# Kernel optimization log

Hardware: AMD Instinct MI355X
Metric: run time of the kernel (lower is better)

The kernel has to match this reference:

```python
import jax, jax.numpy as jnp
import numpy as np

T_MIN, T_MAX = 0.03, 0.34
STEPS = 32
K_MAX = 2
N_DIMS = 2  # homology dimensions [0, 1]

B, C, H, W = 128, 64, 64, 64
P = 128  # persistence pairs per (b, c)


def setup_inputs() -> dict:
    key = jax.random.key(0)
    k1, k2, k3, k4 = jax.random.split(key, 4)
    x = jax.random.uniform(k1, (B, C, H, W), dtype=jnp.float32)
    birth_idx = jax.random.randint(k2, (B, C, P), 0, H * W)
    death_idx = jax.random.randint(k3, (B, C, P), 0, H * W)
    pair_dim = jax.random.randint(k4, (B, C, P), 0, N_DIMS)
    return {"x": x, "birth_idx": birth_idx, "death_idx": death_idx, "pair_dim": pair_dim}


def reference(x, birth_idx, death_idx, pair_dim):
    # x: [B, C, H, W]; indices: [B, C, P] into flattened H*W grid.
    tseq = jnp.linspace(T_MIN, T_MAX, STEPS).astype(x.dtype)  # [T]
    b_, c_, h_, w_ = x.shape
    xf = x.reshape(b_, c_, h_ * w_)
    births = jnp.take_along_axis(xf, birth_idx, axis=-1)  # [B, C, P]
    deaths = jnp.take_along_axis(xf, death_idx, axis=-1)  # [B, C, P]
    # Landscape triangle functions: max(min(t - birth, death - t), 0) -> [B, C, P, T]
    tri = jnp.maximum(jnp.minimum(tseq - births[..., None], deaths[..., None] - tseq), 0.0)
    # Mask pairs by their homology dimension -> [B, C, D, P, T]
    dims = jnp.arange(N_DIMS)
    mask = pair_dim[:, :, None, :, None] == dims[None, None, :, None, None]
    land = jnp.where(mask, tri[:, :, None, :, :], 0.0)
    # Top-K_max landscapes over pairs, per (dim, t): original does -sort(-land)[:K]
    land_t = jnp.swapaxes(land, -1, -2)  # [B, C, D, T, P]
    top, _ = jax.lax.top_k(land_t, K_MAX)  # [B, C, D, T, K]
    return jnp.swapaxes(top, -1, -2)  # [B, C, D, K, T]
```

## Files before the change

### kernel.cpp

```cpp
#include <hip/hip_runtime.h>


constexpr int P = 128;
constexpr float T_MIN = 0.03f;
constexpr float T_MAX = 0.34f;
constexpr float BIG = 1e30f;

__global__ __launch_bounds__(256) void pl_topk_kernel(
    const float* __restrict__ x,
    const int* __restrict__ birth_idx,
    const int* __restrict__ death_idx,
    const int* __restrict__ pair_dim,
    float* __restrict__ out)
{
    __shared__ float2 tab[4][2][P];

    const int lane = threadIdx.x & 63;
    const int w = threadIdx.x >> 6;
    const int wid = blockIdx.x * 4 + w;

    const int d_lane = lane >> 5;
    const int t_idx = lane & 31;
    const float t = T_MIN + (T_MAX - T_MIN) * (float)t_idx * (1.0f / 31.0f);

    const long pbase = (long)wid * P;
    const int bi0 = birth_idx[pbase + lane];
    const int bi1 = birth_idx[pbase + 64 + lane];
    const int di0 = death_idx[pbase + lane];
    const int di1 = death_idx[pbase + 64 + lane];
    const int dm0 = pair_dim[pbase + lane];
    const int dm1 = pair_dim[pbase + 64 + lane];

    const long xbase = (long)wid * 4096;
    const float xb0 = x[xbase + bi0];
    const float xb1 = x[xbase + bi1];
    const float xd0 = x[xbase + di0];
    const float xd1 = x[xbase + di1];

    tab[w][dm0][lane]          = make_float2(xb0, xd0);
    tab[w][1 - dm0][lane]      = make_float2(BIG, -BIG);
    tab[w][dm1][64 + lane]     = make_float2(xb1, xd1);
    tab[w][1 - dm1][64 + lane] = make_float2(BIG, -BIG);

    __syncthreads();

    float m1 = 0.0f, m2 = 0.0f;
    const float2* tp = &tab[w][d_lane][0];
    #pragma unroll
    for (int p = 0; p < P; p += 2) {
        const float4 e = *reinterpret_cast<const float4*>(&tp[p]);
        const float v0 = fminf(t - e.x, e.y - t);
        const float v1 = fminf(t - e.z, e.w - t);
        m2 = fmaxf(m2, fminf(m1, v0));
        m1 = fmaxf(m1, v0);
        m2 = fmaxf(m2, fminf(m1, v1));
        m1 = fmaxf(m1, v1);
    }

    float* o = out + (long)wid * 128;
    o[d_lane * 64 + t_idx] = m1;
    o[d_lane * 64 + 32 + t_idx] = m2;
}

extern "C" void kernel_launch(void* const* d_in, const int* in_sizes, int n_in,
                              void* d_out, int out_size, void* d_ws, size_t ws_size,
                              hipStream_t stream) {
    const float* x = (const float*)d_in[0];
    const int* birth_idx = (const int*)d_in[1];
    const int* death_idx = (const int*)d_in[2];
    const int* pair_dim = (const int*)d_in[3];
    float* out = (float*)d_out;

    dim3 grid(2048), block(256);
    hipLaunchKernelGGL(pl_topk_kernel, grid, block, 0, stream,
                       x, birth_idx, death_idx, pair_dim, out);
}
```

Before: 27.23 us.

## Compact pairs per homology dimension with ballot prefix sums, drop block barrier

Pairs are no longer written into both dimension tables with sentinel padding. A wave ballot and popcount prefix sum now packs each dimension's pairs contiguously, so each half-wave scans only its own pairs (about half of P) instead of all P. The block-wide __syncthreads is replaced by an LDS waitcnt, which relies on each wave only reading its own slice. Index loads become int2 vector loads. The trade-off is a runtime loop bound with reduced unrolling and some extra ballot and popcount work. Correctness also depends on wave-level LDS ordering holding without a barrier.

```diff
diff --git a/kernel.cpp b/kernel.cpp
--- a/kernel.cpp
+++ b/kernel.cpp
@@ -13,7 +13,7 @@
     const int* __restrict__ pair_dim,
     float* __restrict__ out)
 {
-    __shared__ float2 tab[4][2][P];
+    __shared__ float2 tab[4][2][130];
 
     const int lane = threadIdx.x & 63;
     const int w = threadIdx.x >> 6;
@@ -24,30 +24,45 @@
     const float t = T_MIN + (T_MAX - T_MIN) * (float)t_idx * (1.0f / 31.0f);
 
     const long pbase = (long)wid * P;
-    const int bi0 = birth_idx[pbase + lane];
-    const int bi1 = birth_idx[pbase + 64 + lane];
-    const int di0 = death_idx[pbase + lane];
-    const int di1 = death_idx[pbase + 64 + lane];
-    const int dm0 = pair_dim[pbase + lane];
-    const int dm1 = pair_dim[pbase + 64 + lane];
+    const int2 bi = *reinterpret_cast<const int2*>(&birth_idx[pbase + 2 * lane]);
+    const int2 di = *reinterpret_cast<const int2*>(&death_idx[pbase + 2 * lane]);
+    const int2 dm = *reinterpret_cast<const int2*>(&pair_dim[pbase + 2 * lane]);
 
     const long xbase = (long)wid * 4096;
-    const float xb0 = x[xbase + bi0];
-    const float xb1 = x[xbase + bi1];
-    const float xd0 = x[xbase + di0];
-    const float xd1 = x[xbase + di1];
+    const float xb0 = x[xbase + bi.x];
+    const float xb1 = x[xbase + bi.y];
+    const float xd0 = x[xbase + di.x];
+    const float xd1 = x[xbase + di.y];
 
-    tab[w][dm0][lane]          = make_float2(xb0, xd0);
-    tab[w][1 - dm0][lane]      = make_float2(BIG, -BIG);
-    tab[w][dm1][64 + lane]     = make_float2(xb1, xd1);
-    tab[w][1 - dm1][64 + lane] = make_float2(BIG, -BIG);
+    const unsigned long long below = (lane == 63) ? ~0ull >> 1
+                                                  : (1ull << lane) - 1ull;
+    const unsigned long long a_d1 = __ballot(dm.x == 1);
+    const unsigned long long b_d1 = __ballot(dm.y == 1);
+    const unsigned long long a_d0 = ~a_d1;
+    const unsigned long long b_d0 = ~b_d1;
 
-    __syncthreads();
+    const int nA0 = __popcll(a_d0);
+    const int nA1 = 64 - nA0;
+    const int n0 = nA0 + __popcll(b_d0);
+    const int n1 = P - n0;
 
+    const unsigned long long myA = dm.x ? a_d1 : a_d0;
+    const int posA = __popcll(myA & below);
+    const unsigned long long myB = dm.y ? b_d1 : b_d0;
+    const int posB = (dm.y ? nA1 : nA0) + __popcll(myB & below);
+
+    tab[w][dm.x][posA] = make_float2(xb0, xd0);
+    tab[w][dm.y][posB] = make_float2(xb1, xd1);
+    if (lane == 0) tab[w][0][n0] = make_float2(BIG, -BIG);
+    if (lane == 1) tab[w][1][n1] = make_float2(BIG, -BIG);
+
+    asm volatile("s_waitcnt lgkmcnt(0)" ::: "memory");
+
+    const int n_mine = d_lane ? n1 : n0;
     float m1 = 0.0f, m2 = 0.0f;
     const float2* tp = &tab[w][d_lane][0];
-    #pragma unroll
-    for (int p = 0; p < P; p += 2) {
+    #pragma unroll 2
+    for (int p = 0; p < n_mine; p += 2) {
         const float4 e = *reinterpret_cast<const float4*>(&tp[p]);
         const float v0 = fminf(t - e.x, e.y - t);
         const float v1 = fminf(t - e.z, e.w - t);
```

Result: faster. 26.14 us, median of 2 (-4.0%).

## Compact pairs per homology dim via ballot and process two slices per wave

Applied to the files above, without the earlier changes.

Each wave now handles two (b,c) slices. Instead of filling the table with padding sentinels, it uses ballot/popcount to compact pairs by dimension, so each half-wave scans only its own dimension's pairs, about half as many. Index loads become int2-vectorised and the __syncthreads is replaced by an lgkmcnt wait, since each wave uses only its own table slice. The trade-offs are a data-dependent loop trip count, a sentinel entry for odd counts, half the grid size, and more ballot and popcount work.

```diff
diff --git a/kernel.cpp b/kernel.cpp
--- a/kernel.cpp
+++ b/kernel.cpp
@@ -13,53 +13,106 @@
     const int* __restrict__ pair_dim,
     float* __restrict__ out)
 {
-    __shared__ float2 tab[4][2][P];
+    __shared__ float2 tab[4][2][2][130];
 
     const int lane = threadIdx.x & 63;
     const int w = threadIdx.x >> 6;
-    const int wid = blockIdx.x * 4 + w;
+    const int gid = blockIdx.x * 4 + w;
+    const int wid0 = 2 * gid;
 
     const int d_lane = lane >> 5;
     const int t_idx = lane & 31;
     const float t = T_MIN + (T_MAX - T_MIN) * (float)t_idx * (1.0f / 31.0f);
 
-    const long pbase = (long)wid * P;
-    const int bi0 = birth_idx[pbase + lane];
-    const int bi1 = birth_idx[pbase + 64 + lane];
-    const int di0 = death_idx[pbase + lane];
-    const int di1 = death_idx[pbase + 64 + lane];
-    const int dm0 = pair_dim[pbase + lane];
-    const int dm1 = pair_dim[pbase + 64 + lane];
+    const long pb0 = (long)wid0 * P;
+    const long pb1 = pb0 + P;
+    const int2 biA = *reinterpret_cast<const int2*>(&birth_idx[pb0 + 2 * lane]);
+    const int2 biB = *reinterpret_cast<const int2*>(&birth_idx[pb1 + 2 * lane]);
+    const int2 diA = *reinterpret_cast<const int2*>(&death_idx[pb0 + 2 * lane]);
+    const int2 diB = *reinterpret_cast<const int2*>(&death_idx[pb1 + 2 * lane]);
+    const int2 dmA = *reinterpret_cast<const int2*>(&pair_dim[pb0 + 2 * lane]);
+    const int2 dmB = *reinterpret_cast<const int2*>(&pair_dim[pb1 + 2 * lane]);
 
-    const long xbase = (long)wid * 4096;
-    const float xb0 = x[xbase + bi0];
-    const float xb1 = x[xbase + bi1];
-    const float xd0 = x[xbase + di0];
-    const float xd1 = x[xbase + di1];
+    const long xb0 = (long)wid0 * 4096;
+    const long xb1 = xb0 + 4096;
+    const float vA_b0 = x[xb0 + biA.x];
+    const float vA_b1 = x[xb0 + biA.y];
+    const float vA_d0 = x[xb0 + diA.x];
+    const float vA_d1 = x[xb0 + diA.y];
+    const float vB_b0 = x[xb1 + biB.x];
+    const float vB_b1 = x[xb1 + biB.y];
+    const float vB_d0 = x[xb1 + diB.x];
+    const float vB_d1 = x[xb1 + diB.y];
 
-    tab[w][dm0][lane]          = make_float2(xb0, xd0);
-    tab[w][1 - dm0][lane]      = make_float2(BIG, -BIG);
-    tab[w][dm1][64 + lane]     = make_float2(xb1, xd1);
-    tab[w][1 - dm1][64 + lane] = make_float2(BIG, -BIG);
+    const unsigned long long below = (lane == 63) ? ~0ull >> 1
+                                                  : (1ull << lane) - 1ull;
+    const unsigned long long aA1 = __ballot(dmA.x == 1);
+    const unsigned long long bA1 = __ballot(dmA.y == 1);
+    const int nA_a0 = __popcll(~aA1);
+    const int nA_a1 = 64 - nA_a0;
+    const int nA0 = nA_a0 + __popcll(~bA1);
+    const int nA1 = P - nA0;
+    const int posAa = __popcll((dmA.x ? aA1 : ~aA1) & below);
+    const int posAb = (dmA.y ? nA_a1 : nA_a0) + __popcll((dmA.y ? bA1 : ~bA1) & below);
+    const unsigned long long aB1 = __ballot(dmB.x == 1);
+    const unsigned long long bB1 = __ballot(dmB.y == 1);
+    const int nB_a0 = __popcll(~aB1);
+    const int nB_a1 = 64 - nB_a0;
+    const int nB0 = nB_a0 + __popcll(~bB1);
+    const int nB1 = P - nB0;
+    const int posBa = __popcll((dmB.x ? aB1 : ~aB1) & below);
+    const int posBb = (dmB.y ? nB_a1 : nB_a0) + __popcll((dmB.y ? bB1 : ~bB1) & below);
 
-    __syncthreads();
-
-    float m1 = 0.0f, m2 = 0.0f;
-    const float2* tp = &tab[w][d_lane][0];
-    #pragma unroll
-    for (int p = 0; p < P; p += 2) {
-        const float4 e = *reinterpret_cast<const float4*>(&tp[p]);
-        const float v0 = fminf(t - e.x, e.y - t);
-        const float v1 = fminf(t - e.z, e.w - t);
-        m2 = fmaxf(m2, fminf(m1, v0));
-        m1 = fmaxf(m1, v0);
-        m2 = fmaxf(m2, fminf(m1, v1));
-        m1 = fmaxf(m1, v1);
+    tab[w][0][dmA.x][posAa] = make_float2(vA_b0, vA_d0);
+    tab[w][0][dmA.y][posAb] = make_float2(vA_b1, vA_d1);
+    tab[w][1][dmB.x][posBa] = make_float2(vB_b0, vB_d0);
+    tab[w][1][dmB.y][posBb] = make_float2(vB_b1, vB_d1);
+    if (lane < 4) {
+        const int s = lane >> 1, d = lane & 1;
+        const int n = s ? (d ? nB1 : nB0) : (d ? nA1 : nA0);
+        tab[w][s][d][n] = make_float2(BIG, -BIG);
     }
 
-    float* o = out + (long)wid * 128;
-    o[d_lane * 64 + t_idx] = m1;
-    o[d_lane * 64 + 32 + t_idx] = m2;
+    asm volatile("s_waitcnt lgkmcnt(0)" ::: "memory");
+
+    const int nMine0 = d_lane ? nA1 : nA0;
+    const int nMine1 = d_lane ? nB1 : nB0;
+
+    float m1a = 0.0f, m2a = 0.0f;
+    {
+        const float2* tp = &tab[w][0][d_lane][0];
+        #pragma unroll 2
+        for (int p = 0; p < nMine0; p += 2) {
+            const float4 e = *reinterpret_cast<const float4*>(&tp[p]);
+            const float v0 = fminf(t - e.x, e.y - t);
+            const float v1 = fminf(t - e.z, e.w - t);
+            m2a = fmaxf(m2a, fminf(m1a, v0));
+            m1a = fmaxf(m1a, v0);
+            m2a = fmaxf(m2a, fminf(m1a, v1));
+            m1a = fmaxf(m1a, v1);
+        }
+    }
+    float m1b = 0.0f, m2b = 0.0f;
+    {
+        const float2* tp = &tab[w][1][d_lane][0];
+        #pragma unroll 2
+        for (int p = 0; p < nMine1; p += 2) {
+            const float4 e = *reinterpret_cast<const float4*>(&tp[p]);
+            const float v0 = fminf(t - e.x, e.y - t);
+            const float v1 = fminf(t - e.z, e.w - t);
+            m2b = fmaxf(m2b, fminf(m1b, v0));
+            m1b = fmaxf(m1b, v0);
+            m2b = fmaxf(m2b, fminf(m1b, v1));
+            m1b = fmaxf(m1b, v1);
+        }
+    }
+
+    float* o0 = out + (long)wid0 * 128;
+    o0[d_lane * 64 + t_idx] = m1a;
+    o0[d_lane * 64 + 32 + t_idx] = m2a;
+    float* o1 = o0 + 128;
+    o1[d_lane * 64 + t_idx] = m1b;
+    o1[d_lane * 64 + 32 + t_idx] = m2b;
 }
 
 extern "C" void kernel_launch(void* const* d_in, const int* in_sizes, int n_in,
@@ -71,7 +124,7 @@
     const int* pair_dim = (const int*)d_in[3];
     float* out = (float*)d_out;
 
-    dim3 grid(2048), block(256);
+    dim3 grid(1024), block(256);
     hipLaunchKernelGGL(pl_topk_kernel, grid, block, 0, stream,
                        x, birth_idx, death_idx, pair_dim, out);
 }
```

After: 27.63 us. About the same (+1.5%).

## Stage full x slice in LDS with coalesced loads, one block per slice

Applied to the files above, without the earlier changes.

Each block now loads its entire 4096-float slice of x into shared memory with coalesced float4 reads, then gathers birth/death values from LDS instead of doing scattered global loads. The top-2 scan is split across four threads per (dim,t) with shuffle-based merging, and the grid is expanded to one block per (b,c). This aims to replace inefficient random global gathers with streaming reads, at the cost of 16KB LDS per block and possibly reading lines that the gathers would not have touched.

```diff
diff --git a/kernel.cpp b/kernel.cpp
--- a/kernel.cpp
+++ b/kernel.cpp
@@ -13,53 +13,70 @@
     const int* __restrict__ pair_dim,
     float* __restrict__ out)
 {
-    __shared__ float2 tab[4][2][P];
+    __shared__ float sl[4096];
+    __shared__ float2 tab[2][P];
 
-    const int lane = threadIdx.x & 63;
-    const int w = threadIdx.x >> 6;
-    const int wid = blockIdx.x * 4 + w;
+    const int tid = threadIdx.x;
+    const int wid = blockIdx.x;
 
-    const int d_lane = lane >> 5;
-    const int t_idx = lane & 31;
-    const float t = T_MIN + (T_MAX - T_MIN) * (float)t_idx * (1.0f / 31.0f);
+    const float4* xs = reinterpret_cast<const float4*>(x + (long)wid * 4096);
+    float4 v4[4];
+    #pragma unroll
+    for (int c = 0; c < 4; ++c) v4[c] = xs[c * 256 + tid];
 
-    const long pbase = (long)wid * P;
-    const int bi0 = birth_idx[pbase + lane];
-    const int bi1 = birth_idx[pbase + 64 + lane];
-    const int di0 = death_idx[pbase + lane];
-    const int di1 = death_idx[pbase + 64 + lane];
-    const int dm0 = pair_dim[pbase + lane];
-    const int dm1 = pair_dim[pbase + 64 + lane];
+    int bi = 0, di = 0, dmv = 0;
+    if (tid < P) {
+        const long pb = (long)wid * P;
+        bi = birth_idx[pb + tid];
+        di = death_idx[pb + tid];
+        dmv = pair_dim[pb + tid];
+    }
 
-    const long xbase = (long)wid * 4096;
-    const float xb0 = x[xbase + bi0];
-    const float xb1 = x[xbase + bi1];
-    const float xd0 = x[xbase + di0];
-    const float xd1 = x[xbase + di1];
-
-    tab[w][dm0][lane]          = make_float2(xb0, xd0);
-    tab[w][1 - dm0][lane]      = make_float2(BIG, -BIG);
-    tab[w][dm1][64 + lane]     = make_float2(xb1, xd1);
-    tab[w][1 - dm1][64 + lane] = make_float2(BIG, -BIG);
-
+    #pragma unroll
+    for (int c = 0; c < 4; ++c)
+        *reinterpret_cast<float4*>(&sl[(c * 256 + tid) * 4]) = v4[c];
     __syncthreads();
 
+    if (tid < P) {
+        const float xb = sl[bi];
+        const float xd = sl[di];
+        tab[dmv][tid] = make_float2(xb, xd);
+        tab[1 - dmv][tid] = make_float2(BIG, -BIG);
+    }
+    __syncthreads();
+
+    const int q = tid & 3;
+    const int s = tid >> 2;
+    const int d = s >> 5;
+    const int ti = s & 31;
+    const float t = T_MIN + (T_MAX - T_MIN) * (float)ti * (1.0f / 31.0f);
+
     float m1 = 0.0f, m2 = 0.0f;
-    const float2* tp = &tab[w][d_lane][0];
-    #pragma unroll
-    for (int p = 0; p < P; p += 2) {
-        const float4 e = *reinterpret_cast<const float4*>(&tp[p]);
-        const float v0 = fminf(t - e.x, e.y - t);
-        const float v1 = fminf(t - e.z, e.w - t);
-        m2 = fmaxf(m2, fminf(m1, v0));
-        m1 = fmaxf(m1, v0);
-        m2 = fmaxf(m2, fminf(m1, v1));
-        m1 = fmaxf(m1, v1);
+    #pragma unroll 8
+    for (int i = 0; i < 32; ++i) {
+        const float2 e = tab[d][4 * i + q];
+        const float v = fminf(t - e.x, e.y - t);
+        m2 = fmaxf(m2, fminf(m1, v));
+        m1 = fmaxf(m1, v);
+    }
+    {
+        const float o1 = __shfl_xor(m1, 1, 64);
+        const float o2 = __shfl_xor(m2, 1, 64);
+        m2 = fmaxf(fmaxf(m2, o2), fminf(m1, o1));
+        m1 = fmaxf(m1, o1);
+    }
+    {
+        const float o1 = __shfl_xor(m1, 2, 64);
+        const float o2 = __shfl_xor(m2, 2, 64);
+        m2 = fmaxf(fmaxf(m2, o2), fminf(m1, o1));
+        m1 = fmaxf(m1, o1);
     }
 
-    float* o = out + (long)wid * 128;
-    o[d_lane * 64 + t_idx] = m1;
-    o[d_lane * 64 + 32 + t_idx] = m2;
+    if (q == 0) {
+        float* o = out + (long)wid * 128;
+        o[d * 64 + ti] = m1;
+        o[d * 64 + 32 + ti] = m2;
+    }
 }
 
 extern "C" void kernel_launch(void* const* d_in, const int* in_sizes, int n_in,
@@ -71,7 +88,7 @@
     const int* pair_dim = (const int*)d_in[3];
     float* out = (float*)d_out;
 
-    dim3 grid(2048), block(256);
+    dim3 grid(8192), block(256);
     hipLaunchKernelGGL(pl_topk_kernel, grid, block, 0, stream,
                        x, birth_idx, death_idx, pair_dim, out);
 }
```

Result: no change. 27.74 us (+1.9%).
